# Performance work log

Measured on AMD Instinct MI355X. Metric: run time of the kernel, lower is better.

## Reference

```python
import jax, jax.numpy as jnp
import numpy as np

B, T, D, H, L, F, V = 2, 512, 512, 8, 6, 2048, 32000
EPS = 1e-6


def _ln(x, g, b):
    m = x.mean(-1, keepdims=True)
    v = ((x - m) ** 2).mean(-1, keepdims=True)
    return (x - m) / jnp.sqrt(v + EPS) * g + b


def _mha(qx, kx, qkv_w, qkv_b, ow, ob, mask):
    # Wide heads: each head has dim D (Linear(D, H*D) projections, Linear(H*D, D) output).
    Bq, Tq, _ = qx.shape
    def proj(xx, w, bi):
        return (xx @ w + bi).reshape(Bq, Tq, H, D).transpose(0, 2, 1, 3)  # (B,H,T,D)
    q = proj(qx, qkv_w[0], qkv_b[0])
    k = proj(kx, qkv_w[1], qkv_b[1])
    v = proj(kx, qkv_w[2], qkv_b[2])
    s = jnp.einsum('bhqd,bhkd->bhqk', q, k) / jnp.sqrt(jnp.float32(D))
    if mask is not None:
        s = jnp.where(mask, s, -jnp.inf)
    w = jax.nn.softmax(s, axis=-1)
    o = jnp.einsum('bhqk,bhkd->bhqd', w, v).transpose(0, 2, 1, 3).reshape(Bq, Tq, H * D)
    return o @ ow + ob


def _pe(t, d):
    pos = jnp.arange(t, dtype=jnp.float32)[:, None]
    wl = jnp.exp(jnp.arange(0, d, 2, dtype=jnp.float32) / d * -jnp.log(10000.0))
    pe = jnp.zeros((t, d), dtype=jnp.float32)
    pe = pe.at[:, 0::2].set(jnp.sin(pos * wl))
    pe = pe.at[:, 1::2].set(jnp.cos(pos * wl))
    return pe


def _forward(x, y, enc_emb, dec_emb, enc_qkv_w, enc_qkv_b, enc_out_w, enc_out_b,
             enc_ln1_g, enc_ln1_b, enc_ff_w1, enc_ff_b1, enc_ff_w2, enc_ff_b2,
             enc_ln2_g, enc_ln2_b, dec_sa_qkv_w, dec_sa_qkv_b, dec_sa_out_w, dec_sa_out_b,
             dec_ln1_g, dec_ln1_b, dec_ca_qkv_w, dec_ca_qkv_b, dec_ca_out_w, dec_ca_out_b,
             dec_ln2_g, dec_ln2_b, dec_ff_w1, dec_ff_b1, dec_ff_w2, dec_ff_b2,
             dec_ln3_g, dec_ln3_b, head_w, head_b):
    pe = _pe(T, D)
    scale = jnp.sqrt(jnp.float32(D))
    # ---- encoder ----
    h = enc_emb[x] * scale + pe  # (B,T,D)
    for i in range(L):
        a = _mha(h, h, enc_qkv_w[i], enc_qkv_b[i], enc_out_w[i], enc_out_b[i], None)
        h = _ln(a + h, enc_ln1_g[i], enc_ln1_b[i])
        f = jax.nn.relu(h @ enc_ff_w1[i] + enc_ff_b1[i]) @ enc_ff_w2[i] + enc_ff_b2[i]
        h = _ln(f + h, enc_ln2_g[i], enc_ln2_b[i])
    # ---- decoder ----
    causal = jnp.tril(jnp.ones((T, T), dtype=bool))[None, None]  # (1,1,T,T)
    d = dec_emb[y] * scale + pe
    for i in range(L):
        a = _mha(d, d, dec_sa_qkv_w[i], dec_sa_qkv_b[i], dec_sa_out_w[i], dec_sa_out_b[i], causal)
        d = _ln(a + d, dec_ln1_g[i], dec_ln1_b[i])
        c = _mha(d, h, dec_ca_qkv_w[i], dec_ca_qkv_b[i], dec_ca_out_w[i], dec_ca_out_b[i], None)
        d = _ln(c + d, dec_ln2_g[i], dec_ln2_b[i])
        f = jax.nn.relu(d @ dec_ff_w1[i] + dec_ff_b1[i]) @ dec_ff_w2[i] + dec_ff_b2[i]
        d = _ln(f + d, dec_ln3_g[i], dec_ln3_b[i])
    return d @ head_w + head_b  # (B,T,V) logits


def setup_inputs() -> dict:
    key = jax.random.key(0)
    ks = iter(jax.random.split(key, 40))
    def nrm(shape):
        return jax.random.normal(next(ks), shape, dtype=jnp.float32) * 0.02
    HD = H * D
    return {
        'x': jax.random.randint(next(ks), (B, T), 0, V, dtype=jnp.int32),
        'y': jax.random.randint(next(ks), (B, T), 0, V, dtype=jnp.int32),
        'enc_emb': nrm((V, D)), 'dec_emb': nrm((V, D)),
        'enc_qkv_w': nrm((L, 3, D, HD)), 'enc_qkv_b': jnp.zeros((L, 3, HD)),
        'enc_out_w': nrm((L, HD, D)), 'enc_out_b': jnp.zeros((L, D)),
        'enc_ln1_g': jnp.ones((L, D)), 'enc_ln1_b': jnp.zeros((L, D)),
        'enc_ff_w1': nrm((L, D, F)), 'enc_ff_b1': jnp.zeros((L, F)),
        'enc_ff_w2': nrm((L, F, D)), 'enc_ff_b2': jnp.zeros((L, D)),
        'enc_ln2_g': jnp.ones((L, D)), 'enc_ln2_b': jnp.zeros((L, D)),
        'dec_sa_qkv_w': nrm((L, 3, D, HD)), 'dec_sa_qkv_b': jnp.zeros((L, 3, HD)),
        'dec_sa_out_w': nrm((L, HD, D)), 'dec_sa_out_b': jnp.zeros((L, D)),
        'dec_ln1_g': jnp.ones((L, D)), 'dec_ln1_b': jnp.zeros((L, D)),
        'dec_ca_qkv_w': nrm((L, 3, D, HD)), 'dec_ca_qkv_b': jnp.zeros((L, 3, HD)),
        'dec_ca_out_w': nrm((L, HD, D)), 'dec_ca_out_b': jnp.zeros((L, D)),
        'dec_ln2_g': jnp.ones((L, D)), 'dec_ln2_b': jnp.zeros((L, D)),
        'dec_ff_w1': nrm((L, D, F)), 'dec_ff_b1': jnp.zeros((L, F)),
        'dec_ff_w2': nrm((L, F, D)), 'dec_ff_b2': jnp.zeros((L, D)),
        'dec_ln3_g': jnp.ones((L, D)), 'dec_ln3_b': jnp.zeros((L, D)),
        'head_w': nrm((D, V)), 'head_b': jnp.zeros((V,)),
    }


def reference(x, y, enc_emb, dec_emb, enc_qkv_w, enc_qkv_b, enc_out_w, enc_out_b,
              enc_ln1_g, enc_ln1_b, enc_ff_w1, enc_ff_b1, enc_ff_w2, enc_ff_b2,
              enc_ln2_g, enc_ln2_b, dec_sa_qkv_w, dec_sa_qkv_b, dec_sa_out_w, dec_sa_out_b,
              dec_ln1_g, dec_ln1_b, dec_ca_qkv_w, dec_ca_qkv_b, dec_ca_out_w, dec_ca_out_b,
              dec_ln2_g, dec_ln2_b, dec_ff_w1, dec_ff_b1, dec_ff_w2, dec_ff_b2,
              dec_ln3_g, dec_ln3_b, head_w, head_b):
    return _forward(x, y, enc_emb, dec_emb, enc_qkv_w, enc_qkv_b, enc_out_w, enc_out_b,
                    enc_ln1_g, enc_ln1_b, enc_ff_w1, enc_ff_b1, enc_ff_w2, enc_ff_b2,
                    enc_ln2_g, enc_ln2_b, dec_sa_qkv_w, dec_sa_qkv_b, dec_sa_out_w, dec_sa_out_b,
                    dec_ln1_g, dec_ln1_b, dec_ca_qkv_w, dec_ca_qkv_b, dec_ca_out_w, dec_ca_out_b,
                    dec_ln2_g, dec_ln2_b, dec_ff_w1, dec_ff_b1, dec_ff_w2, dec_ff_b2,
                    dec_ln3_g, dec_ln3_b, head_w, head_b)
```

## Files before the change

### kernel.cpp

```cpp
#include <hip/hip_runtime.h>
#include <hip/hip_bf16.h>

#define B_ 2
#define T_ 512
#define D_ 512
#define H_ 8
#define L_ 6
#define F_ 2048
#define V_ 32000
#define BT_ (B_ * T_)
#define HD_ (H_ * D_)
#define BH_ (B_ * H_)

typedef __attribute__((ext_vector_type(8))) short short8;
typedef __attribute__((ext_vector_type(4))) short short4v;
typedef __attribute__((ext_vector_type(4))) float f32x4;

__device__ __forceinline__ short f2b(float f) {
  __hip_bfloat16 h = __float2bfloat16(f);
  short u; __builtin_memcpy(&u, &h, 2); return u;
}
__device__ __forceinline__ void store_c(float* p, float v) { *p = v; }
__device__ __forceinline__ void store_c(short* p, float v) { *p = f2b(v); }

__global__ __launch_bounds__(256) void embed_kernel(
    const int* __restrict__ tok, const float* __restrict__ emb,
    float* __restrict__ out, short* __restrict__ out16)
{
  const int row = blockIdx.x;
  const int t = row & (T_ - 1);
  const int token = tok[row];
  const float* e = emb + (size_t)token * D_;
  float* o = out + (size_t)row * D_;
  short* o16 = out16 + (size_t)row * D_;
  const float scale = sqrtf((float)D_);
  const float nl = -logf(10000.0f);
  for (int d = threadIdx.x; d < D_; d += 256) {
    int i = d >> 1;
    float wl = expf(nl * (2.0f * (float)i) / (float)D_);
    float ang = (float)t * wl;
    float pe = (d & 1) ? cosf(ang) : sinf(ang);
    float v = e[d] * scale + pe;
    o[d] = v; o16[d] = f2b(v);
  }
}

template<bool BTM, typename OutT, int BM>
__global__ __launch_bounds__(256, 3) void mfma_gemm(
    const short* __restrict__ A, long lda, long a_hi, long a_lo,
    const void* __restrict__ Bv, long ldb, long b_hi, long b_lo,
    OutT* __restrict__ C, long ldc, long c_hi, long c_lo, long pstride,
    short* __restrict__ Ct, int trans_hh,
    int K, int nh, int ksplit, float scale,
    const float* __restrict__ bias, long bias_stride)
{
  constexpr int SA = BM + 1;
  constexpr int AU = BM / 32;
  constexpr int WRN = (BM == 128) ? 2 : 1;
  constexpr int WN  = 128 / (4 / WRN);
  constexpr int NR  = WN / 16;
  __shared__ short8 As8[8 * SA];
  __shared__ short8 Bs8[8 * 129];
  const int tid = threadIdx.x;
  const int bh = blockIdx.z / ksplit;
  const int kz = blockIdx.z - bh * ksplit;
  const int bb = bh / nh, hh = bh - bb * nh;
  const short* Ab = A + (long)bb * a_hi + (long)hh * a_lo;
  const short* Bbs = (const short*)Bv + (long)bb * b_hi + (long)hh * b_lo;
  const float* Bbf = (const float*)Bv + (long)bb * b_hi + (long)hh * b_lo;
  OutT* Cb = C + (long)bb * c_hi + (long)hh * c_lo + (long)kz * pstride;

  const int gx = gridDim.x, gy = gridDim.y;
  const int nwg = gx * gy;
  int lin = blockIdx.y * gx + blockIdx.x;
  {
    const int xcd = lin & 7, idx = lin >> 3;
    const int q = nwg >> 3, r = nwg & 7;
    lin = (xcd < r ? xcd * (q + 1) : r * (q + 1) + (xcd - r) * q) + idx;
  }
  const int bn = (lin / gy) * 128;
  const int bm = (lin % gy) * BM;

  const int klen = K / ksplit, kbase = kz * klen;
  const int lane = tid & 63, wid = tid >> 6;
  const int wr = (WRN == 2) ? (wid >> 1) : 0;
  const int wc = (WRN == 2) ? (wid & 1) : wid;
  const int lg = lane >> 4, r16 = lane & 15;

  int arow[AU], acol[AU];
#pragma unroll
  for (int u = 0; u < AU; ++u) { int o = u * 256 + tid; arow[u] = o >> 3; acol[u] = o & 7; }
  const int ncol = tid & 127, nsh = tid >> 7;

  short8 pa[AU];
  short8 pbt[4];
  float  pbn[4][8];

  auto load = [&](int k0) {
#pragma unroll
    for (int u = 0; u < AU; ++u)
      pa[u] = *(const short8*)(Ab + (long)(bm + arow[u]) * lda + (k0 + acol[u] * 8));
    if constexpr (BTM) {
#pragma unroll
      for (int u = 0; u < 4; ++u)
        pbt[u] = *(const short8*)(Bbs + (long)(bn + (u * 256 + tid) / 8) * ldb + (k0 + ((u * 256 + tid) & 7) * 8));
    } else {
      const float* s = Bbf + (long)(k0 + nsh * 32) * ldb + (bn + ncol);
#pragma unroll
      for (int i = 0; i < 4; ++i)
#pragma unroll
        for (int j = 0; j < 8; ++j)
          pbn[i][j] = s[(long)(i * 8 + j) * ldb];
    }
  };
  auto stage = [&]() {
#pragma unroll
    for (int u = 0; u < AU; ++u) As8[acol[u] * SA + arow[u]] = pa[u];
    if constexpr (BTM) {
#pragma unroll
      for (int u = 0; u < 4; ++u)
        Bs8[((u * 256 + tid) & 7) * 129 + (u * 256 + tid) / 8] = pbt[u];
    } else {
#pragma unroll
      for (int i = 0; i < 4; ++i) {
        short8 v;
#pragma unroll
        for (int j = 0; j < 8; ++j) v[j] = f2b(pbn[i][j]);
        Bs8[(nsh * 4 + i) * 129 + ncol] = v;
      }
    }
  };

  f32x4 acc[4][NR] = {};
  auto domfma = [&]() {
#pragma unroll
    for (int kb = 0; kb < 2; ++kb) {
      const int cha = (kb * 4 + lg) * SA;
      const int chb = (kb * 4 + lg) * 129;
      short8 a0 = As8[cha + wr * 64 +  0 + r16];
      short8 a1 = As8[cha + wr * 64 + 16 + r16];
      short8 a2 = As8[cha + wr * 64 + 32 + r16];
      short8 a3 = As8[cha + wr * 64 + 48 + r16];
#pragma unroll
      for (int n = 0; n < NR; ++n) {
        short8 bfr = Bs8[chb + wc * WN + n * 16 + r16];
        acc[0][n] = __builtin_amdgcn_mfma_f32_16x16x32_bf16(a0, bfr, acc[0][n], 0, 0, 0);
        acc[1][n] = __builtin_amdgcn_mfma_f32_16x16x32_bf16(a1, bfr, acc[1][n], 0, 0, 0);
        acc[2][n] = __builtin_amdgcn_mfma_f32_16x16x32_bf16(a2, bfr, acc[2][n], 0, 0, 0);
        acc[3][n] = __builtin_amdgcn_mfma_f32_16x16x32_bf16(a3, bfr, acc[3][n], 0, 0, 0);
      }
    }
  };

  load(kbase);
  stage();
  __syncthreads();
  const int nsteps = klen >> 6;
  for (int t = 0; t < nsteps; ++t) {
    const bool more = (t + 1 < nsteps);
    if (more) load(kbase + (t + 1) * 64);
    domfma();
    if (more) { __syncthreads(); stage(); __syncthreads(); }
  }

  const float* bp = bias ? bias + (long)hh * bias_stride : nullptr;
  if (hh == trans_hh) {
#pragma unroll
    for (int m = 0; m < 4; ++m)
#pragma unroll
      for (int n = 0; n < NR; ++n) {
        const int col = bn + wc * WN + n * 16 + r16;
        const float badd = bp ? bp[col] : 0.0f;
        short4v sv;
#pragma unroll
        for (int rr = 0; rr < 4; ++rr) sv[rr] = f2b(acc[m][n][rr] * scale + badd);
        *(short4v*)(Ct + (long)col * BT_ + (bm + wr * 64 + m * 16 + lg * 4)) = sv;
      }
  } else {
#pragma unroll
    for (int m = 0; m < 4; ++m)
#pragma unroll
      for (int rr = 0; rr < 4; ++rr) {
        const int row = bm + wr * 64 + m * 16 + lg * 4 + rr;
        OutT* crow = Cb + (long)row * ldc + bn + wc * WN + r16;
#pragma unroll
        for (int n = 0; n < NR; ++n) {
          float v = acc[m][n][rr] * scale;
          if (bp) v += bp[bn + wc * WN + n * 16 + r16];
          store_c(&crow[n * 16], v);
        }
      }
  }
}

__global__ __launch_bounds__(256) void reduce_bias_relu_bf16(
    const float* __restrict__ P, long pstride, int ks,
    const float* __restrict__ bias, short* __restrict__ out, long mn, int N)
{
  const long i = ((long)blockIdx.x * 256 + threadIdx.x) * 4;
  if (i >= mn) return;
  float4 s = *(const float4*)(P + i);
  for (int z = 1; z < ks; ++z) {
    float4 t = *(const float4*)(P + (long)z * pstride + i);
    s.x += t.x; s.y += t.y; s.z += t.z; s.w += t.w;
  }
  const int col = (int)(i % N);
  s.x += bias[col]; s.y += bias[col + 1]; s.z += bias[col + 2]; s.w += bias[col + 3];
  short4v o;
  o[0] = f2b(fmaxf(s.x, 0.f)); o[1] = f2b(fmaxf(s.y, 0.f));
  o[2] = f2b(fmaxf(s.z, 0.f)); o[3] = f2b(fmaxf(s.w, 0.f));
  *(short4v*)(out + i) = o;
}

__global__ __launch_bounds__(256) void reduce_ln_kernel(
    const float* __restrict__ P, long pstride, int ks,
    const float* __restrict__ bias, float* __restrict__ hbuf, short* __restrict__ h16,
    const float* __restrict__ gam, const float* __restrict__ bet)
{
  __shared__ float red[256];
  const int row = blockIdx.x, tid = threadIdx.x;
  const long base = (long)row * D_;
  float s0 = hbuf[base + tid] + bias[tid];
  float s1 = hbuf[base + tid + 256] + bias[tid + 256];
  for (int z = 0; z < ks; ++z) {
    s0 += P[(long)z * pstride + base + tid];
    s1 += P[(long)z * pstride + base + tid + 256];
  }
  red[tid] = s0 + s1; __syncthreads();
  for (int o = 128; o > 0; o >>= 1) { if (tid < o) red[tid] += red[tid + o]; __syncthreads(); }
  const float mean = red[0] * (1.0f / D_); __syncthreads();
  const float d0 = s0 - mean, d1 = s1 - mean;
  red[tid] = d0 * d0 + d1 * d1; __syncthreads();
  for (int o = 128; o > 0; o >>= 1) { if (tid < o) red[tid] += red[tid + o]; __syncthreads(); }
  const float inv = rsqrtf(red[0] * (1.0f / D_) + 1e-6f);
  const float v0 = d0 * inv * gam[tid] + bet[tid];
  const float v1 = d1 * inv * gam[tid + 256] + bet[tid + 256];
  hbuf[base + tid] = v0;       h16[base + tid] = f2b(v0);
  hbuf[base + tid + 256] = v1; h16[base + tid + 256] = f2b(v1);
}

__global__ __launch_bounds__(256) void softmax_kernel(
    const float* __restrict__ S, short* __restrict__ P, int causal)
{
  __shared__ float red[256];
  const int q = blockIdx.x, bh = blockIdx.y, tid = threadIdx.x;
  const float* row = S + ((size_t)bh * T_ + q) * T_;
  short* prow = P + ((size_t)bh * T_ + q) * T_;
  const int n = causal ? (q + 1) : T_;
  const float v0 = row[tid], v1 = row[tid + 256];
  const bool in0 = tid < n, in1 = (tid + 256) < n;
  red[tid] = fmaxf(in0 ? v0 : -3.0e38f, in1 ? v1 : -3.0e38f);
  __syncthreads();
  for (int o = 128; o > 0; o >>= 1) { if (tid < o) red[tid] = fmaxf(red[tid], red[tid + o]); __syncthreads(); }
  const float m = red[0]; __syncthreads();
  const float e0 = in0 ? expf(v0 - m) : 0.0f;
  const float e1 = in1 ? expf(v1 - m) : 0.0f;
  red[tid] = e0 + e1; __syncthreads();
  for (int o = 128; o > 0; o >>= 1) { if (tid < o) red[tid] += red[tid + o]; __syncthreads(); }
  const float inv = 1.0f / red[0];
  prow[tid] = f2b(e0 * inv);
  prow[tid + 256] = f2b(e1 * inv);
}

extern "C" void kernel_launch(void* const* d_in, const int* in_sizes, int n_in,
                              void* d_out, int out_size, void* d_ws, size_t ws_size,
                              hipStream_t stream)
{
  const int*   x         = (const int*)d_in[0];
  const int*   y         = (const int*)d_in[1];
  const float* enc_emb   = (const float*)d_in[2];
  const float* dec_emb   = (const float*)d_in[3];
  const float* enc_qkv_w = (const float*)d_in[4];
  const float* enc_qkv_b = (const float*)d_in[5];
  const float* enc_out_w = (const float*)d_in[6];
  const float* enc_out_b = (const float*)d_in[7];
  const float* enc_ln1_g = (const float*)d_in[8];
  const float* enc_ln1_b = (const float*)d_in[9];
  const float* enc_ff_w1 = (const float*)d_in[10];
  const float* enc_ff_b1 = (const float*)d_in[11];
  const float* enc_ff_w2 = (const float*)d_in[12];
  const float* enc_ff_b2 = (const float*)d_in[13];
  const float* enc_ln2_g = (const float*)d_in[14];
  const float* enc_ln2_b = (const float*)d_in[15];
  const float* dec_sa_qkv_w = (const float*)d_in[16];
  const float* dec_sa_qkv_b = (const float*)d_in[17];
  const float* dec_sa_out_w = (const float*)d_in[18];
  const float* dec_sa_out_b = (const float*)d_in[19];
  const float* dec_ln1_g = (const float*)d_in[20];
  const float* dec_ln1_b = (const float*)d_in[21];
  const float* dec_ca_qkv_w = (const float*)d_in[22];
  const float* dec_ca_qkv_b = (const float*)d_in[23];
  const float* dec_ca_out_w = (const float*)d_in[24];
  const float* dec_ca_out_b = (const float*)d_in[25];
  const float* dec_ln2_g = (const float*)d_in[26];
  const float* dec_ln2_b = (const float*)d_in[27];
  const float* dec_ff_w1 = (const float*)d_in[28];
  const float* dec_ff_b1 = (const float*)d_in[29];
  const float* dec_ff_w2 = (const float*)d_in[30];
  const float* dec_ff_b2 = (const float*)d_in[31];
  const float* dec_ln3_g = (const float*)d_in[32];
  const float* dec_ln3_b = (const float*)d_in[33];
  const float* head_w    = (const float*)d_in[34];
  const float* head_b    = (const float*)d_in[35];
  float* out = (float*)d_out;

  char* wsb = (char*)d_ws;
  size_t off = 0;
  auto carve = [&](size_t bytes) { char* p = wsb + off; off += (bytes + 255) & ~255ull; return p; };
  float* h    = (float*)carve((size_t)BT_ * D_ * 4);
  float* dd   = (float*)carve((size_t)BT_ * D_ * 4);
  short* hb16 = (short*)carve((size_t)BT_ * D_ * 2);
  short* db16 = (short*)carve((size_t)BT_ * D_ * 2);
  short* Qb   = (short*)carve((size_t)BT_ * HD_ * 2);
  short* Kb   = (short*)carve((size_t)BT_ * HD_ * 2);
  short* Vt   = (short*)carve((size_t)HD_ * BT_ * 2);
  float* Sb   = (float*)carve((size_t)BH_ * T_ * T_ * 4);
  short* Pb   = (short*)carve((size_t)BH_ * T_ * T_ * 2);
  short* Ob   = Qb;
  short* mid  = Qb;
  (void)ws_size;

  dim3 blk(256);
  const long TT  = (long)T_ * T_;
  const long THD = (long)T_ * HD_;
  const long WQKV = (long)D_ * HD_;

  auto gemm = [&](bool bt, bool of32, bool bm64,
                  const short* A, long lda, long a_hi, long a_lo,
                  const void* Bp, long ldb, long b_hi, long b_lo,
                  void* Cp, long ldc, long c_hi, long c_lo, long pstride,
                  short* Ct, int trans_hh,
                  int M, int N, int K, int batch, int nh, int ksplit,
                  float scale, const float* bias, long bstride) {
    dim3 grd(N / 128, M / (bm64 ? 64 : 128), batch * ksplit);
    if (bm64) {
      if (bt) {
        if (of32) mfma_gemm<true , float, 64><<<grd, blk, 0, stream>>>(A, lda, a_hi, a_lo, Bp, ldb, b_hi, b_lo,
            (float*)Cp, ldc, c_hi, c_lo, pstride, Ct, trans_hh, K, nh, ksplit, scale, bias, bstride);
        else      mfma_gemm<true , short, 64><<<grd, blk, 0, stream>>>(A, lda, a_hi, a_lo, Bp, ldb, b_hi, b_lo,
            (short*)Cp, ldc, c_hi, c_lo, pstride, Ct, trans_hh, K, nh, ksplit, scale, bias, bstride);
      } else {
        if (of32) mfma_gemm<false, float, 64><<<grd, blk, 0, stream>>>(A, lda, a_hi, a_lo, Bp, ldb, b_hi, b_lo,
            (float*)Cp, ldc, c_hi, c_lo, pstride, Ct, trans_hh, K, nh, ksplit, scale, bias, bstride);
        else      mfma_gemm<false, short, 64><<<grd, blk, 0, stream>>>(A, lda, a_hi, a_lo, Bp, ldb, b_hi, b_lo,
            (short*)Cp, ldc, c_hi, c_lo, pstride, Ct, trans_hh, K, nh, ksplit, scale, bias, bstride);
      }
    } else {
      if (of32) mfma_gemm<false, float, 128><<<grd, blk, 0, stream>>>(A, lda, a_hi, a_lo, Bp, ldb, b_hi, b_lo,
          (float*)Cp, ldc, c_hi, c_lo, pstride, Ct, trans_hh, K, nh, ksplit, scale, bias, bstride);
      else      mfma_gemm<false, short, 128><<<grd, blk, 0, stream>>>(A, lda, a_hi, a_lo, Bp, ldb, b_hi, b_lo,
          (short*)Cp, ldc, c_hi, c_lo, pstride, Ct, trans_hh, K, nh, ksplit, scale, bias, bstride);
    }
  };

  auto attention = [&](const short* qsrc, const short* kvsrc, bool self,
                       const float* qkvw, const float* qkvb,
                       const float* ow, const float* ob,
                       float* resid, short* resid16, int causal,
                       const float* lng, const float* lnb) {
    if (self) {
      gemm(false, false, true, qsrc, D_, 0, 0, qkvw, HD_, 0, WQKV,
           Qb, HD_, 0, (long)(Kb - Qb), 0, Vt, 2,
           BT_, HD_, D_, 3, 3, 1, 1.0f, qkvb, HD_);
    } else {
      gemm(false, false, true, qsrc, D_, 0, 0, qkvw, HD_, 0, 0,
           Qb, HD_, 0, 0, 0, nullptr, -1,
           BT_, HD_, D_, 1, 1, 1, 1.0f, qkvb, 0);
      gemm(false, false, true, kvsrc, D_, 0, 0, qkvw + WQKV, HD_, 0, WQKV,
           Kb, HD_, 0, 0, 0, Vt, 1,
           BT_, HD_, D_, 2, 2, 1, 1.0f, qkvb + HD_, HD_);
    }
    gemm(true, true, true, Qb, HD_, THD, D_, Kb, HD_, THD, D_,
         Sb, T_, (long)H_ * TT, TT, 0, nullptr, -1,
         T_, T_, D_, BH_, H_, 1, 0.044194173824159216f, nullptr, 0);
    softmax_kernel<<<dim3(T_, BH_), blk, 0, stream>>>(Sb, Pb, causal);
    gemm(true, false, true, Pb, T_, (long)H_ * TT, TT, Vt, BT_, T_, (long)D_ * BT_,
         Ob, HD_, THD, D_, 0, nullptr, -1,
         T_, D_, T_, BH_, H_, 1, 1.0f, nullptr, 0);
    gemm(false, true, true, Ob, HD_, 0, 0, ow, D_, 0, 0,
         Sb, D_, 0, 0, (long)BT_ * D_, nullptr, -1,
         BT_, D_, HD_, 1, 1, 8, 1.0f, nullptr, 0);
    reduce_ln_kernel<<<dim3(BT_), blk, 0, stream>>>(
        Sb, (long)BT_ * D_, 8, ob, resid, resid16, lng, lnb);
  };

  auto ffn = [&](float* resid, short* resid16,
                 const float* w1, const float* b1,
                 const float* w2, const float* b2,
                 const float* lng, const float* lnb) {
    gemm(false, true, true, resid16, D_, 0, 0, w1, F_, 0, 0,
         Sb, F_, 0, 0, (long)BT_ * F_, nullptr, -1,
         BT_, F_, D_, 1, 1, 2, 1.0f, nullptr, 0);
    reduce_bias_relu_bf16<<<dim3(BT_ * F_ / 1024), blk, 0, stream>>>(
        Sb, (long)BT_ * F_, 2, b1, mid, (long)BT_ * F_, F_);
    gemm(false, true, true, mid, F_, 0, 0, w2, D_, 0, 0,
         Sb, D_, 0, 0, (long)BT_ * D_, nullptr, -1,
         BT_, D_, F_, 1, 1, 8, 1.0f, nullptr, 0);
    reduce_ln_kernel<<<dim3(BT_), blk, 0, stream>>>(
        Sb, (long)BT_ * D_, 8, b2, resid, resid16, lng, lnb);
  };

  embed_kernel<<<dim3(BT_), blk, 0, stream>>>(x, enc_emb, h, hb16);
  for (int i = 0; i < L_; ++i) {
    attention(hb16, hb16, true,
              enc_qkv_w + (size_t)i * 3 * WQKV, enc_qkv_b + (size_t)i * 3 * HD_,
              enc_out_w + (size_t)i * HD_ * D_, enc_out_b + (size_t)i * D_,
              h, hb16, 0, enc_ln1_g + (size_t)i * D_, enc_ln1_b + (size_t)i * D_);
    ffn(h, hb16, enc_ff_w1 + (size_t)i * D_ * F_, enc_ff_b1 + (size_t)i * F_,
        enc_ff_w2 + (size_t)i * F_ * D_, enc_ff_b2 + (size_t)i * D_,
        enc_ln2_g + (size_t)i * D_, enc_ln2_b + (size_t)i * D_);
  }

  embed_kernel<<<dim3(BT_), blk, 0, stream>>>(y, dec_emb, dd, db16);
  for (int i = 0; i < L_; ++i) {
    attention(db16, db16, true,
              dec_sa_qkv_w + (size_t)i * 3 * WQKV, dec_sa_qkv_b + (size_t)i * 3 * HD_,
              dec_sa_out_w + (size_t)i * HD_ * D_, dec_sa_out_b + (size_t)i * D_,
              dd, db16, 1, dec_ln1_g + (size_t)i * D_, dec_ln1_b + (size_t)i * D_);
    attention(db16, hb16, false,
              dec_ca_qkv_w + (size_t)i * 3 * WQKV, dec_ca_qkv_b + (size_t)i * 3 * HD_,
              dec_ca_out_w + (size_t)i * HD_ * D_, dec_ca_out_b + (size_t)i * D_,
              dd, db16, 0, dec_ln2_g + (size_t)i * D_, dec_ln2_b + (size_t)i * D_);
    ffn(dd, db16, dec_ff_w1 + (size_t)i * D_ * F_, dec_ff_b1 + (size_t)i * F_,
        dec_ff_w2 + (size_t)i * F_ * D_, dec_ff_b2 + (size_t)i * D_,
        dec_ln3_g + (size_t)i * D_, dec_ln3_b + (size_t)i * D_);
  }

  gemm(false, true, false, db16, D_, 0, 0, head_w, V_, 0, 0,
       out, V_, 0, 0, 0, nullptr, -1,
       BT_, V_, D_, 1, 1, 1, 1.0f, head_b, 0);
}
```

Measured before the change: 2.392 ms.

## Double-buffer GEMM tiles in LDS with async global_load_lds and XOR swizzle

Rewrites the GEMM main loop so A tiles, and B tiles in the transposed-B case, are copied straight from global memory into LDS with global_load_lds. Two LDS buffers let the next tile load while MFMAs run on the current one, removing one barrier and the register-staging round trip. The padded LDS layout is replaced by an XOR swizzle to avoid bank conflicts. It also adds an unused relu flag and lowers the occupancy hint for BM=128, while doubling LDS use per block, which may cut occupancy.

```diff
diff --git a/kernel.cpp b/kernel.cpp
--- a/kernel.cpp
+++ b/kernel.cpp
@@ -22,6 +22,12 @@
 }
 __device__ __forceinline__ void store_c(float* p, float v) { *p = v; }
 __device__ __forceinline__ void store_c(short* p, float v) { *p = f2b(v); }
+
+__device__ __forceinline__ void gload16(const void* g, void* l) {
+  __builtin_amdgcn_global_load_lds(
+      (const __attribute__((address_space(1))) void*)g,
+      (__attribute__((address_space(3))) void*)l, 16, 0, 0);
+}
 
 __global__ __launch_bounds__(256) void embed_kernel(
     const int* __restrict__ tok, const float* __restrict__ emb,
@@ -46,21 +52,21 @@
 }
 
 template<bool BTM, typename OutT, int BM>
-__global__ __launch_bounds__(256, 3) void mfma_gemm(
+__global__ __launch_bounds__(256, BM == 128 ? 2 : 3) void mfma_gemm(
     const short* __restrict__ A, long lda, long a_hi, long a_lo,
     const void* __restrict__ Bv, long ldb, long b_hi, long b_lo,
     OutT* __restrict__ C, long ldc, long c_hi, long c_lo, long pstride,
-    short* __restrict__ Ct, int trans_hh,
+    short* __restrict__ Ct, int trans_hh, int relu,
     int K, int nh, int ksplit, float scale,
     const float* __restrict__ bias, long bias_stride)
 {
-  constexpr int SA = BM + 1;
-  constexpr int AU = BM / 32;
   constexpr int WRN = (BM == 128) ? 2 : 1;
-  constexpr int WN  = 128 / (4 / WRN);
+  constexpr int WN  = (BM == 128) ? 64 : 32;
   constexpr int NR  = WN / 16;
-  __shared__ short8 As8[8 * SA];
-  __shared__ short8 Bs8[8 * 129];
+  constexpr int CA  = BM / 32;
+  constexpr int PA  = BM * 8;
+  __shared__ short8 AsL[2 * PA];
+  __shared__ short8 BsL[2 * 1024];
   const int tid = threadIdx.x;
   const int bh = blockIdx.z / ksplit;
   const int kz = blockIdx.z - bh * ksplit;
@@ -82,68 +88,66 @@
   const int bm = (lin % gy) * BM;
 
   const int klen = K / ksplit, kbase = kz * klen;
-  const int lane = tid & 63, wid = tid >> 6;
-  const int wr = (WRN == 2) ? (wid >> 1) : 0;
-  const int wc = (WRN == 2) ? (wid & 1) : wid;
+  const int lane = tid & 63, w4 = tid >> 6;
+  const int wr = (WRN == 2) ? (w4 >> 1) : 0;
+  const int wc = (WRN == 2) ? (w4 & 1) : w4;
   const int lg = lane >> 4, r16 = lane & 15;
-
-  int arow[AU], acol[AU];
-#pragma unroll
-  for (int u = 0; u < AU; ++u) { int o = u * 256 + tid; arow[u] = o >> 3; acol[u] = o & 7; }
   const int ncol = tid & 127, nsh = tid >> 7;
 
-  short8 pa[AU];
-  short8 pbt[4];
-  float  pbn[4][8];
-
-  auto load = [&](int k0) {
-#pragma unroll
-    for (int u = 0; u < AU; ++u)
-      pa[u] = *(const short8*)(Ab + (long)(bm + arow[u]) * lda + (k0 + acol[u] * 8));
-    if constexpr (BTM) {
-#pragma unroll
-      for (int u = 0; u < 4; ++u)
-        pbt[u] = *(const short8*)(Bbs + (long)(bn + (u * 256 + tid) / 8) * ldb + (k0 + ((u * 256 + tid) & 7) * 8));
-    } else {
-      const float* s = Bbf + (long)(k0 + nsh * 32) * ldb + (bn + ncol);
-#pragma unroll
-      for (int i = 0; i < 4; ++i)
-#pragma unroll
-        for (int j = 0; j < 8; ++j)
-          pbn[i][j] = s[(long)(i * 8 + j) * ldb];
-    }
-  };
-  auto stage = [&]() {
-#pragma unroll
-    for (int u = 0; u < AU; ++u) As8[acol[u] * SA + arow[u]] = pa[u];
-    if constexpr (BTM) {
-#pragma unroll
-      for (int u = 0; u < 4; ++u)
-        Bs8[((u * 256 + tid) & 7) * 129 + (u * 256 + tid) / 8] = pbt[u];
-    } else {
-#pragma unroll
-      for (int i = 0; i < 4; ++i) {
-        short8 v;
-#pragma unroll
-        for (int j = 0; j < 8; ++j) v[j] = f2b(pbn[i][j]);
-        Bs8[(nsh * 4 + i) * 129 + ncol] = v;
-      }
+  float pbn[4][8];
+
+  auto issueA = [&](int k0, int bo) {
+#pragma unroll
+    for (int u = 0; u < CA; ++u) {
+      const int p = (w4 * CA + u) * 64 + lane;
+      const int row = p >> 3, c = p & 7;
+      const int cs = c ^ (row & 7);
+      gload16(Ab + (long)(bm + row) * lda + (k0 + cs * 8),
+              &AsL[bo + (w4 * CA + u) * 64]);
+    }
+  };
+  auto issueB = [&](int k0, int bo) {
+#pragma unroll
+    for (int u = 0; u < 4; ++u) {
+      const int p = (w4 * 4 + u) * 64 + lane;
+      const int col = p >> 3, c = p & 7;
+      const int cs = c ^ (col & 7);
+      gload16(Bbs + (long)(bn + col) * ldb + (k0 + cs * 8),
+              &BsL[bo + (w4 * 4 + u) * 64]);
+    }
+  };
+  auto loadBn = [&](int k0) {
+    const float* s = Bbf + (long)(k0 + nsh * 32) * ldb + (bn + ncol);
+#pragma unroll
+    for (int i = 0; i < 4; ++i)
+#pragma unroll
+      for (int j = 0; j < 8; ++j)
+        pbn[i][j] = s[(long)(i * 8 + j) * ldb];
+  };
+  auto stageBn = [&](int bo) {
+#pragma unroll
+    for (int i = 0; i < 4; ++i) {
+      const int cc = nsh * 4 + i;
+      short8 v;
+#pragma unroll
+      for (int j = 0; j < 8; ++j) v[j] = f2b(pbn[i][j]);
+      BsL[bo + ncol * 8 + (cc ^ (ncol & 7))] = v;
     }
   };
 
   f32x4 acc[4][NR] = {};
-  auto domfma = [&]() {
+  auto domfma = [&](int abo, int bbo) {
 #pragma unroll
     for (int kb = 0; kb < 2; ++kb) {
-      const int cha = (kb * 4 + lg) * SA;
-      const int chb = (kb * 4 + lg) * 129;
-      short8 a0 = As8[cha + wr * 64 +  0 + r16];
-      short8 a1 = As8[cha + wr * 64 + 16 + r16];
-      short8 a2 = As8[cha + wr * 64 + 32 + r16];
-      short8 a3 = As8[cha + wr * 64 + 48 + r16];
+      const int ch = kb * 4 + lg;
+      const int swz = ch ^ (r16 & 7);
+      short8 a0 = AsL[abo + (wr * 64 +  0 + r16) * 8 + swz];
+      short8 a1 = AsL[abo + (wr * 64 + 16 + r16) * 8 + swz];
+      short8 a2 = AsL[abo + (wr * 64 + 32 + r16) * 8 + swz];
+      short8 a3 = AsL[abo + (wr * 64 + 48 + r16) * 8 + swz];
 #pragma unroll
       for (int n = 0; n < NR; ++n) {
-        short8 bfr = Bs8[chb + wc * WN + n * 16 + r16];
+        short8 bfr = BsL[bbo + (wc * WN + n * 16 + r16) * 8 + swz];
         acc[0][n] = __builtin_amdgcn_mfma_f32_16x16x32_bf16(a0, bfr, acc[0][n], 0, 0, 0);
         acc[1][n] = __builtin_amdgcn_mfma_f32_16x16x32_bf16(a1, bfr, acc[1][n], 0, 0, 0);
         acc[2][n] = __builtin_amdgcn_mfma_f32_16x16x32_bf16(a2, bfr, acc[2][n], 0, 0, 0);
@@ -152,15 +156,25 @@
     }
   };
 
-  load(kbase);
-  stage();
+  issueA(kbase, 0);
+  if constexpr (BTM) { issueB(kbase, 0); }
+  else               { loadBn(kbase); stageBn(0); }
   __syncthreads();
+
   const int nsteps = klen >> 6;
   for (int t = 0; t < nsteps; ++t) {
     const bool more = (t + 1 < nsteps);
-    if (more) load(kbase + (t + 1) * 64);
-    domfma();
-    if (more) { __syncthreads(); stage(); __syncthreads(); }
+    const int cur = t & 1, nxt = cur ^ 1;
+    if (more) {
+      issueA(kbase + (t + 1) * 64, nxt * PA);
+      if constexpr (BTM) issueB(kbase + (t + 1) * 64, nxt * 1024);
+      else               loadBn(kbase + (t + 1) * 64);
+    }
+    domfma(cur * PA, cur * 1024);
+    if (more) {
+      if constexpr (!BTM) stageBn(nxt * 1024);
+      __syncthreads();
+    }
   }
 
   const float* bp = bias ? bias + (long)hh * bias_stride : nullptr;
@@ -187,6 +201,7 @@
         for (int n = 0; n < NR; ++n) {
           float v = acc[m][n][rr] * scale;
           if (bp) v += bp[bn + wc * WN + n * 16 + r16];
+          if (relu) v = fmaxf(v, 0.0f);
           store_c(&crow[n * 16], v);
         }
       }
@@ -325,7 +340,7 @@
   const long THD = (long)T_ * HD_;
   const long WQKV = (long)D_ * HD_;
 
-  auto gemm = [&](bool bt, bool of32, bool bm64,
+  auto gemm = [&](bool bt, bool of32, bool bm64, int relu,
                   const short* A, long lda, long a_hi, long a_lo,
                   const void* Bp, long ldb, long b_hi, long b_lo,
                   void* Cp, long ldc, long c_hi, long c_lo, long pstride,
@@ -336,20 +351,20 @@
     if (bm64) {
       if (bt) {
         if (of32) mfma_gemm<true , float, 64><<<grd, blk, 0, stream>>>(A, lda, a_hi, a_lo, Bp, ldb, b_hi, b_lo,
-            (float*)Cp, ldc, c_hi, c_lo, pstride, Ct, trans_hh, K, nh, ksplit, scale, bias, bstride);
+            (float*)Cp, ldc, c_hi, c_lo, pstride, Ct, trans_hh, relu, K, nh, ksplit, scale, bias, bstride);
         else      mfma_gemm<true , short, 64><<<grd, blk, 0, stream>>>(A, lda, a_hi, a_lo, Bp, ldb, b_hi, b_lo,
-            (short*)Cp, ldc, c_hi, c_lo, pstride, Ct, trans_hh, K, nh, ksplit, scale, bias, bstride);
+            (short*)Cp, ldc, c_hi, c_lo, pstride, Ct, trans_hh, relu, K, nh, ksplit, scale, bias, bstride);
       } else {
         if (of32) mfma_gemm<false, float, 64><<<grd, blk, 0, stream>>>(A, lda, a_hi, a_lo, Bp, ldb, b_hi, b_lo,
-            (float*)Cp, ldc, c_hi, c_lo, pstride, Ct, trans_hh, K, nh, ksplit, scale, bias, bstride);
+            (float*)Cp, ldc, c_hi, c_lo, pstride, Ct, trans_hh, relu, K, nh, ksplit, scale, bias, bstride);
         else      mfma_gemm<false, short, 64><<<grd, blk, 0, stream>>>(A, lda, a_hi, a_lo, Bp, ldb, b_hi, b_lo,
-            (short*)Cp, ldc, c_hi, c_lo, pstride, Ct, trans_hh, K, nh, ksplit, scale, bias, bstride);
+            (short*)Cp, ldc, c_hi, c_lo, pstride, Ct, trans_hh, relu, K, nh, ksplit, scale, bias, bstride);
       }
     } else {
       if (of32) mfma_gemm<false, float, 128><<<grd, blk, 0, stream>>>(A, lda, a_hi, a_lo, Bp, ldb, b_hi, b_lo,
-          (float*)Cp, ldc, c_hi, c_lo, pstride, Ct, trans_hh, K, nh, ksplit, scale, bias, bstride);
+          (float*)Cp, ldc, c_hi, c_lo, pstride, Ct, trans_hh, relu, K, nh, ksplit, scale, bias, bstride);
       else      mfma_gemm<false, short, 128><<<grd, blk, 0, stream>>>(A, lda, a_hi, a_lo, Bp, ldb, b_hi, b_lo,
-          (short*)Cp, ldc, c_hi, c_lo, pstride, Ct, trans_hh, K, nh, ksplit, scale, bias, bstride);
+          (short*)Cp, ldc, c_hi, c_lo, pstride, Ct, trans_hh, relu, K, nh, ksplit, scale, bias, bstride);
     }
   };
 
@@ -359,25 +374,25 @@
                        float* resid, short* resid16, int causal,
                        const float* lng, const float* lnb) {
     if (self) {
-      gemm(false, false, true, qsrc, D_, 0, 0, qkvw, HD_, 0, WQKV,
+      gemm(false, false, true, 0, qsrc, D_, 0, 0, qkvw, HD_, 0, WQKV,
            Qb, HD_, 0, (long)(Kb - Qb), 0, Vt, 2,
            BT_, HD_, D_, 3, 3, 1, 1.0f, qkvb, HD_);
     } else {
-      gemm(false, false, true, qsrc, D_, 0, 0, qkvw, HD_, 0, 0,
+      gemm(false, false, true, 0, qsrc, D_, 0, 0, qkvw, HD_, 0, 0,
            Qb, HD_, 0, 0, 0, nullptr, -1,
            BT_, HD_, D_, 1, 1, 1, 1.0f, qkvb, 0);
-      gemm(false, false, true, kvsrc, D_, 0, 0, qkvw + WQKV, HD_, 0, WQKV,
+      gemm(false, false, true, 0, kvsrc, D_, 0, 0, qkvw + WQKV, HD_, 0, WQKV,
            Kb, HD_, 0, 0, 0, Vt, 1,
            BT_, HD_, D_, 2, 2, 1, 1.0f, qkvb + HD_, HD_);
     }
-    gemm(true, true, true, Qb, HD_, THD, D_, Kb, HD_, THD, D_,
+    gemm(true, true, true, 0, Qb, HD_, THD, D_, Kb, HD_, THD, D_,
          Sb, T_, (long)H_ * TT, TT, 0, nullptr, -1,
          T_, T_, D_, BH_, H_, 1, 0.044194173824159216f, nullptr, 0);
     softmax_kernel<<<dim3(T_, BH_), blk, 0, stream>>>(Sb, Pb, causal);
-    gemm(true, false, true, Pb, T_, (long)H_ * TT, TT, Vt, BT_, T_, (long)D_ * BT_,
+    gemm(true, false, true, 0, Pb, T_, (long)H_ * TT, TT, Vt, BT_, T_, (long)D_ * BT_,
          Ob, HD_, THD, D_, 0, nullptr, -1,
          T_, D_, T_, BH_, H_, 1, 1.0f, nullptr, 0);
-    gemm(false, true, true, Ob, HD_, 0, 0, ow, D_, 0, 0,
+    gemm(false, true, true, 0, Ob, HD_, 0, 0, ow, D_, 0, 0,
          Sb, D_, 0, 0, (long)BT_ * D_, nullptr, -1,
          BT_, D_, HD_, 1, 1, 8, 1.0f, nullptr, 0);
     reduce_ln_kernel<<<dim3(BT_), blk, 0, stream>>>(
@@ -388,12 +403,12 @@
                  const float* w1, const float* b1,
                  const float* w2, const float* b2,
                  const float* lng, const float* lnb) {
-    gemm(false, true, true, resid16, D_, 0, 0, w1, F_, 0, 0,
+    gemm(false, true, true, 0, resid16, D_, 0, 0, w1, F_, 0, 0,
          Sb, F_, 0, 0, (long)BT_ * F_, nullptr, -1,
          BT_, F_, D_, 1, 1, 2, 1.0f, nullptr, 0);
     reduce_bias_relu_bf16<<<dim3(BT_ * F_ / 1024), blk, 0, stream>>>(
         Sb, (long)BT_ * F_, 2, b1, mid, (long)BT_ * F_, F_);
-    gemm(false, true, true, mid, F_, 0, 0, w2, D_, 0, 0,
+    gemm(false, true, true, 0, mid, F_, 0, 0, w2, D_, 0, 0,
          Sb, D_, 0, 0, (long)BT_ * D_, nullptr, -1,
          BT_, D_, F_, 1, 1, 8, 1.0f, nullptr, 0);
     reduce_ln_kernel<<<dim3(BT_), blk, 0, stream>>>(
@@ -426,7 +441,7 @@
         dec_ln3_g + (size_t)i * D_, dec_ln3_b + (size_t)i * D_);
   }
 
-  gemm(false, true, false, db16, D_, 0, 0, head_w, V_, 0, 0,
+  gemm(false, true, false, 0, db16, D_, 0, 0, head_w, V_, 0, 0,
        out, V_, 0, 0, 0, nullptr, -1,
        BT_, V_, D_, 1, 1, 1, 1.0f, head_b, 0);
 }
```

Result: slower. 2.624 ms (+9.7%).

## Skip masked causal tiles, fuse FFN bias+ReLU into GEMM, merge cross-attn QKV

Applied to the files above, without the earlier changes.

With a causal mask, the QK^T GEMM now returns early on tiles that lie entirely above the diagonal, and the PV GEMM limits its K loop to the causal extent, so masked work is skipped. The first FFN GEMM no longer uses split-K partials followed by a separate reduce kernel; it applies bias and ReLU in its epilogue and writes bf16 directly. Cross-attention Q and K/V projections run as one batched launch, using an a_once offset so head 0 reads the query source and the other heads read the memory source. The cost is more kernel parameters and branches, and the FFN1 GEMM loses split-K parallelism.

```diff
diff --git a/kernel.cpp b/kernel.cpp
--- a/kernel.cpp
+++ b/kernel.cpp
@@ -47,17 +47,17 @@
 
 template<bool BTM, typename OutT, int BM>
 __global__ __launch_bounds__(256, 3) void mfma_gemm(
-    const short* __restrict__ A, long lda, long a_hi, long a_lo,
+    const short* __restrict__ A, long lda, long a_hi, long a_lo, int a_once,
     const void* __restrict__ Bv, long ldb, long b_hi, long b_lo,
     OutT* __restrict__ C, long ldc, long c_hi, long c_lo, long pstride,
-    short* __restrict__ Ct, int trans_hh,
+    short* __restrict__ Ct, int trans_hh, int relu, int cskip, int cklim,
     int K, int nh, int ksplit, float scale,
     const float* __restrict__ bias, long bias_stride)
 {
   constexpr int SA = BM + 1;
   constexpr int AU = BM / 32;
   constexpr int WRN = (BM == 128) ? 2 : 1;
-  constexpr int WN  = 128 / (4 / WRN);
+  constexpr int WN  = (BM == 128) ? 64 : 32;
   constexpr int NR  = WN / 16;
   __shared__ short8 As8[8 * SA];
   __shared__ short8 Bs8[8 * 129];
@@ -65,7 +65,8 @@
   const int bh = blockIdx.z / ksplit;
   const int kz = blockIdx.z - bh * ksplit;
   const int bb = bh / nh, hh = bh - bb * nh;
-  const short* Ab = A + (long)bb * a_hi + (long)hh * a_lo;
+  const long a_off = a_once ? (hh >= 1 ? a_lo : 0) : (long)hh * a_lo;
+  const short* Ab = A + (long)bb * a_hi + a_off;
   const short* Bbs = (const short*)Bv + (long)bb * b_hi + (long)hh * b_lo;
   const float* Bbf = (const float*)Bv + (long)bb * b_hi + (long)hh * b_lo;
   OutT* Cb = C + (long)bb * c_hi + (long)hh * c_lo + (long)kz * pstride;
@@ -80,6 +81,7 @@
   }
   const int bn = (lin / gy) * 128;
   const int bm = (lin % gy) * BM;
+  if (cskip && bn > bm + BM - 1) return;
 
   const int klen = K / ksplit, kbase = kz * klen;
   const int lane = tid & 63, wid = tid >> 6;
@@ -90,6 +92,9 @@
   int arow[AU], acol[AU];
 #pragma unroll
   for (int u = 0; u < AU; ++u) { int o = u * 256 + tid; arow[u] = o >> 3; acol[u] = o & 7; }
+  int brow[4], bcol[4];
+#pragma unroll
+  for (int u = 0; u < 4; ++u) { int o = u * 256 + tid; brow[u] = o >> 3; bcol[u] = o & 7; }
   const int ncol = tid & 127, nsh = tid >> 7;
 
   short8 pa[AU];
@@ -103,7 +108,7 @@
     if constexpr (BTM) {
 #pragma unroll
       for (int u = 0; u < 4; ++u)
-        pbt[u] = *(const short8*)(Bbs + (long)(bn + (u * 256 + tid) / 8) * ldb + (k0 + ((u * 256 + tid) & 7) * 8));
+        pbt[u] = *(const short8*)(Bbs + (long)(bn + brow[u]) * ldb + (k0 + bcol[u] * 8));
     } else {
       const float* s = Bbf + (long)(k0 + nsh * 32) * ldb + (bn + ncol);
 #pragma unroll
@@ -118,8 +123,7 @@
     for (int u = 0; u < AU; ++u) As8[acol[u] * SA + arow[u]] = pa[u];
     if constexpr (BTM) {
 #pragma unroll
-      for (int u = 0; u < 4; ++u)
-        Bs8[((u * 256 + tid) & 7) * 129 + (u * 256 + tid) / 8] = pbt[u];
+      for (int u = 0; u < 4; ++u) Bs8[bcol[u] * 129 + brow[u]] = pbt[u];
     } else {
 #pragma unroll
       for (int i = 0; i < 4; ++i) {
@@ -152,10 +156,11 @@
     }
   };
 
+  int nsteps = klen >> 6;
+  if (cklim) { const int lim = (bm >> 6) + 1; if (lim < nsteps) nsteps = lim; }
   load(kbase);
   stage();
   __syncthreads();
-  const int nsteps = klen >> 6;
   for (int t = 0; t < nsteps; ++t) {
     const bool more = (t + 1 < nsteps);
     if (more) load(kbase + (t + 1) * 64);
@@ -187,29 +192,11 @@
         for (int n = 0; n < NR; ++n) {
           float v = acc[m][n][rr] * scale;
           if (bp) v += bp[bn + wc * WN + n * 16 + r16];
+          if (relu) v = fmaxf(v, 0.0f);
           store_c(&crow[n * 16], v);
         }
       }
   }
-}
-
-__global__ __launch_bounds__(256) void reduce_bias_relu_bf16(
-    const float* __restrict__ P, long pstride, int ks,
-    const float* __restrict__ bias, short* __restrict__ out, long mn, int N)
-{
-  const long i = ((long)blockIdx.x * 256 + threadIdx.x) * 4;
-  if (i >= mn) return;
-  float4 s = *(const float4*)(P + i);
-  for (int z = 1; z < ks; ++z) {
-    float4 t = *(const float4*)(P + (long)z * pstride + i);
-    s.x += t.x; s.y += t.y; s.z += t.z; s.w += t.w;
-  }
-  const int col = (int)(i % N);
-  s.x += bias[col]; s.y += bias[col + 1]; s.z += bias[col + 2]; s.w += bias[col + 3];
-  short4v o;
-  o[0] = f2b(fmaxf(s.x, 0.f)); o[1] = f2b(fmaxf(s.y, 0.f));
-  o[2] = f2b(fmaxf(s.z, 0.f)); o[3] = f2b(fmaxf(s.w, 0.f));
-  *(short4v*)(out + i) = o;
 }
 
 __global__ __launch_bounds__(256) void reduce_ln_kernel(
@@ -325,8 +312,8 @@
   const long THD = (long)T_ * HD_;
   const long WQKV = (long)D_ * HD_;
 
-  auto gemm = [&](bool bt, bool of32, bool bm64,
-                  const short* A, long lda, long a_hi, long a_lo,
+  auto gemm = [&](bool bt, bool of32, bool bm64, int relu, int cskip, int cklim,
+                  const short* A, long lda, long a_hi, long a_lo, int a_once,
                   const void* Bp, long ldb, long b_hi, long b_lo,
                   void* Cp, long ldc, long c_hi, long c_lo, long pstride,
                   short* Ct, int trans_hh,
@@ -335,21 +322,21 @@
     dim3 grd(N / 128, M / (bm64 ? 64 : 128), batch * ksplit);
     if (bm64) {
       if (bt) {
-        if (of32) mfma_gemm<true , float, 64><<<grd, blk, 0, stream>>>(A, lda, a_hi, a_lo, Bp, ldb, b_hi, b_lo,
-            (float*)Cp, ldc, c_hi, c_lo, pstride, Ct, trans_hh, K, nh, ksplit, scale, bias, bstride);
-        else      mfma_gemm<true , short, 64><<<grd, blk, 0, stream>>>(A, lda, a_hi, a_lo, Bp, ldb, b_hi, b_lo,
-            (short*)Cp, ldc, c_hi, c_lo, pstride, Ct, trans_hh, K, nh, ksplit, scale, bias, bstride);
+        if (of32) mfma_gemm<true , float, 64><<<grd, blk, 0, stream>>>(A, lda, a_hi, a_lo, a_once, Bp, ldb, b_hi, b_lo,
+            (float*)Cp, ldc, c_hi, c_lo, pstride, Ct, trans_hh, relu, cskip, cklim, K, nh, ksplit, scale, bias, bstride);
+        else      mfma_gemm<true , short, 64><<<grd, blk, 0, stream>>>(A, lda, a_hi, a_lo, a_once, Bp, ldb, b_hi, b_lo,
+            (short*)Cp, ldc, c_hi, c_lo, pstride, Ct, trans_hh, relu, cskip, cklim, K, nh, ksplit, scale, bias, bstride);
       } else {
-        if (of32) mfma_gemm<false, float, 64><<<grd, blk, 0, stream>>>(A, lda, a_hi, a_lo, Bp, ldb, b_hi, b_lo,
-            (float*)Cp, ldc, c_hi, c_lo, pstride, Ct, trans_hh, K, nh, ksplit, scale, bias, bstride);
-        else      mfma_gemm<false, short, 64><<<grd, blk, 0, stream>>>(A, lda, a_hi, a_lo, Bp, ldb, b_hi, b_lo,
-            (short*)Cp, ldc, c_hi, c_lo, pstride, Ct, trans_hh, K, nh, ksplit, scale, bias, bstride);
+        if (of32) mfma_gemm<false, float, 64><<<grd, blk, 0, stream>>>(A, lda, a_hi, a_lo, a_once, Bp, ldb, b_hi, b_lo,
+            (float*)Cp, ldc, c_hi, c_lo, pstride, Ct, trans_hh, relu, cskip, cklim, K, nh, ksplit, scale, bias, bstride);
+        else      mfma_gemm<false, short, 64><<<grd, blk, 0, stream>>>(A, lda, a_hi, a_lo, a_once, Bp, ldb, b_hi, b_lo,
+            (short*)Cp, ldc, c_hi, c_lo, pstride, Ct, trans_hh, relu, cskip, cklim, K, nh, ksplit, scale, bias, bstride);
       }
     } else {
-      if (of32) mfma_gemm<false, float, 128><<<grd, blk, 0, stream>>>(A, lda, a_hi, a_lo, Bp, ldb, b_hi, b_lo,
-          (float*)Cp, ldc, c_hi, c_lo, pstride, Ct, trans_hh, K, nh, ksplit, scale, bias, bstride);
-      else      mfma_gemm<false, short, 128><<<grd, blk, 0, stream>>>(A, lda, a_hi, a_lo, Bp, ldb, b_hi, b_lo,
-          (short*)Cp, ldc, c_hi, c_lo, pstride, Ct, trans_hh, K, nh, ksplit, scale, bias, bstride);
+      if (of32) mfma_gemm<false, float, 128><<<grd, blk, 0, stream>>>(A, lda, a_hi, a_lo, a_once, Bp, ldb, b_hi, b_lo,
+          (float*)Cp, ldc, c_hi, c_lo, pstride, Ct, trans_hh, relu, cskip, cklim, K, nh, ksplit, scale, bias, bstride);
+      else      mfma_gemm<false, short, 128><<<grd, blk, 0, stream>>>(A, lda, a_hi, a_lo, a_once, Bp, ldb, b_hi, b_lo,
+          (short*)Cp, ldc, c_hi, c_lo, pstride, Ct, trans_hh, relu, cskip, cklim, K, nh, ksplit, scale, bias, bstride);
     }
   };
 
@@ -358,26 +345,19 @@
                        const float* ow, const float* ob,
                        float* resid, short* resid16, int causal,
                        const float* lng, const float* lnb) {
-    if (self) {
-      gemm(false, false, true, qsrc, D_, 0, 0, qkvw, HD_, 0, WQKV,
-           Qb, HD_, 0, (long)(Kb - Qb), 0, Vt, 2,
-           BT_, HD_, D_, 3, 3, 1, 1.0f, qkvb, HD_);
-    } else {
-      gemm(false, false, true, qsrc, D_, 0, 0, qkvw, HD_, 0, 0,
-           Qb, HD_, 0, 0, 0, nullptr, -1,
-           BT_, HD_, D_, 1, 1, 1, 1.0f, qkvb, 0);
-      gemm(false, false, true, kvsrc, D_, 0, 0, qkvw + WQKV, HD_, 0, WQKV,
-           Kb, HD_, 0, 0, 0, Vt, 1,
-           BT_, HD_, D_, 2, 2, 1, 1.0f, qkvb + HD_, HD_);
-    }
-    gemm(true, true, true, Qb, HD_, THD, D_, Kb, HD_, THD, D_,
+    gemm(false, false, true, 0, 0, 0, qsrc, D_, 0, (long)(kvsrc - qsrc), 1,
+         qkvw, HD_, 0, WQKV,
+         Qb, HD_, 0, (long)(Kb - Qb), 0, Vt, 2,
+         BT_, HD_, D_, 3, 3, 1, 1.0f, qkvb, HD_);
+    gemm(true, true, true, 0, causal, 0, Qb, HD_, THD, D_, 0, Kb, HD_, THD, D_,
          Sb, T_, (long)H_ * TT, TT, 0, nullptr, -1,
          T_, T_, D_, BH_, H_, 1, 0.044194173824159216f, nullptr, 0);
     softmax_kernel<<<dim3(T_, BH_), blk, 0, stream>>>(Sb, Pb, causal);
-    gemm(true, false, true, Pb, T_, (long)H_ * TT, TT, Vt, BT_, T_, (long)D_ * BT_,
+    gemm(true, false, true, 0, 0, causal, Pb, T_, (long)H_ * TT, TT, 0,
+         Vt, BT_, T_, (long)D_ * BT_,
          Ob, HD_, THD, D_, 0, nullptr, -1,
          T_, D_, T_, BH_, H_, 1, 1.0f, nullptr, 0);
-    gemm(false, true, true, Ob, HD_, 0, 0, ow, D_, 0, 0,
+    gemm(false, true, true, 0, 0, 0, Ob, HD_, 0, 0, 0, ow, D_, 0, 0,
          Sb, D_, 0, 0, (long)BT_ * D_, nullptr, -1,
          BT_, D_, HD_, 1, 1, 8, 1.0f, nullptr, 0);
     reduce_ln_kernel<<<dim3(BT_), blk, 0, stream>>>(
@@ -388,12 +368,10 @@
                  const float* w1, const float* b1,
                  const float* w2, const float* b2,
                  const float* lng, const float* lnb) {
-    gemm(false, true, true, resid16, D_, 0, 0, w1, F_, 0, 0,
-         Sb, F_, 0, 0, (long)BT_ * F_, nullptr, -1,
-         BT_, F_, D_, 1, 1, 2, 1.0f, nullptr, 0);
-    reduce_bias_relu_bf16<<<dim3(BT_ * F_ / 1024), blk, 0, stream>>>(
-        Sb, (long)BT_ * F_, 2, b1, mid, (long)BT_ * F_, F_);
-    gemm(false, true, true, mid, F_, 0, 0, w2, D_, 0, 0,
+    gemm(false, false, true, 1, 0, 0, resid16, D_, 0, 0, 0, w1, F_, 0, 0,
+         mid, F_, 0, 0, 0, nullptr, -1,
+         BT_, F_, D_, 1, 1, 1, 1.0f, b1, 0);
+    gemm(false, true, true, 0, 0, 0, mid, F_, 0, 0, 0, w2, D_, 0, 0,
          Sb, D_, 0, 0, (long)BT_ * D_, nullptr, -1,
          BT_, D_, F_, 1, 1, 8, 1.0f, nullptr, 0);
     reduce_ln_kernel<<<dim3(BT_), blk, 0, stream>>>(
@@ -426,7 +404,7 @@
         dec_ln3_g + (size_t)i * D_, dec_ln3_b + (size_t)i * D_);
   }
 
-  gemm(false, true, false, db16, D_, 0, 0, head_w, V_, 0, 0,
+  gemm(false, true, false, 0, 0, 0, db16, D_, 0, 0, 0, head_w, V_, 0, 0,
        out, V_, 0, 0, 0, nullptr, -1,
        BT_, V_, D_, 1, 1, 1, 1.0f, head_b, 0);
 }
```

After: 2.350 ms. No clear change (-1.8%).
